# Kernel tuning notes

Hardware: AMD Instinct MI355X
Metric: run time of the kernel (lower is better)

## Reference

```python
import jax, jax.numpy as jnp
import numpy as np
import math

B, H_IM, W_IM, HDIM, HEADS, PS = 16, 56, 56, 512, 8, 7


def setup_inputs() -> dict:
    key = jax.random.key(0)
    ks = jax.random.split(key, 4)
    x = jax.random.normal(ks[0], (B, H_IM * W_IM, HDIM), jnp.float32)
    mask = jnp.zeros((1, 1, H_IM, W_IM), jnp.bool_)
    Wqkv = jax.random.normal(ks[1], (HDIM, 3 * HDIM), jnp.float32) * 0.02
    Wproj = jax.random.normal(ks[2], (HDIM, HDIM), jnp.float32) * 0.02
    bproj = jnp.zeros((HDIM,), jnp.float32)
    rel_bias = jax.random.normal(ks[3], (HEADS, PS * PS, PS * PS), jnp.float32) * 0.02
    return {"x": x, "mask": mask, "Wqkv": Wqkv, "Wproj": Wproj,
            "bproj": bproj, "rel_bias": rel_bias, "H": H_IM, "W": W_IM}


def reference(x, mask, Wqkv, Wproj, bproj, rel_bias, H, W):
    b = x.shape[0]
    ps, g, hd = PS, HEADS, HDIM
    dh = hd // g
    scale = dh ** (-0.5)

    qkv = x @ Wqkv                                   # [b, H*W, 3*hd]
    qkv = qkv.reshape(b, H, W, 3 * hd)
    pad_b = int(math.ceil(H / ps)) * ps - H
    pad_r = int(math.ceil(W / ps)) * ps - W
    qkv = jnp.pad(qkv, ((0, 0), (0, pad_b), (0, pad_r), (0, 0)))
    kmask = jnp.pad(mask, ((0, 0), (0, 0), (0, pad_b), (0, pad_r)), constant_values=True)
    Hp, Wp = H + pad_b, W + pad_r
    sh, sw = Hp // ps, Wp // ps
    K, P = ps * ps, sh * sw

    # patchify: b (sh kh) (sw kw) c -> b (kh kw) (sh sw) c
    qkv = qkv.reshape(b, sh, ps, sw, ps, 3 * hd).transpose(0, 2, 4, 1, 3, 5).reshape(b, K, P, 3 * hd)
    kmask = kmask.reshape(1, 1, sh, ps, sw, ps).transpose(0, 1, 3, 5, 2, 4).reshape(1, 1, K, P)

    qkv = qkv.reshape(b, K, P, 3, g, dh)
    q, k, v = qkv[:, :, :, 0], qkv[:, :, :, 1], qkv[:, :, :, 2]  # each [b, K, P, g, dh]

    attn = jnp.einsum('bqpgc,bkpgc->bgqkp', q, k)    # [b, g, K, K, P]
    attn = (attn + rel_bias[None, :, :, :, None]) * scale
    m = kmask[:, None]                                # [1, 1, 1, K, P]
    attn = jnp.where(m, -jnp.inf, attn)
    attn = jax.nn.softmax(attn, axis=-2)              # softmax over key positions within window
    attn = jnp.where(m, 0.0, attn)

    out = jnp.einsum('bgqkp,bkpgc->bqpgc', attn, v)
    out = out.reshape(b, K, P, hd)
    # un-patchify: b (kh kw) (sh sw) c -> b (sh kh) (sw kw) c
    out = out.reshape(b, ps, ps, sh, sw, hd).transpose(0, 3, 1, 4, 2, 5).reshape(b, Hp, Wp, hd)
    out = out[:, :H, :W, :].reshape(b, H * W, hd)
    return out @ Wproj + bproj
```

## Files before the change

kernel.cpp:

```cpp
#include <hip/hip_runtime.h>
#include <hip/hip_bf16.h>

using bf16 = __hip_bfloat16;
using bf16x8 = __attribute__((ext_vector_type(8))) short;
using f32x4  = __attribute__((ext_vector_type(4))) float;

#define B_    16
#define HIM   56
#define WIM   56
#define HD    512
#define NHEAD 8
#define DH    64
#define NTOK  (HIM*WIM)
#define M_    (B_*NTOK)
#define K49   49

__device__ __forceinline__ void gload_lds16(const void* g, void* l) {
  __builtin_amdgcn_global_load_lds(
      (__attribute__((address_space(1))) const void*)g,
      (__attribute__((address_space(3))) void*)l, 16, 0, 0);
}

__global__ __launch_bounds__(256) void cvt_x_kernel(const float* __restrict__ in,
                                                    bf16* __restrict__ out) {
  size_t i = ((size_t)blockIdx.x * 256 + threadIdx.x) * 8;
  float4 a = *(const float4*)(in + i);
  float4 b = *(const float4*)(in + i + 4);
  union { uint4 v; bf16 h[8]; } o;
  o.h[0] = __float2bfloat16(a.x); o.h[1] = __float2bfloat16(a.y);
  o.h[2] = __float2bfloat16(a.z); o.h[3] = __float2bfloat16(a.w);
  o.h[4] = __float2bfloat16(b.x); o.h[5] = __float2bfloat16(b.y);
  o.h[6] = __float2bfloat16(b.z); o.h[7] = __float2bfloat16(b.w);
  *(uint4*)(out + i) = o.v;
}

__global__ __launch_bounds__(256) void cvt_transpose_kernel(const float* __restrict__ in,
                                                            bf16* __restrict__ out,
                                                            int K, int N) {
  int idx = blockIdx.x * 256 + threadIdx.x;
  int k = idx / N, n = idx - k * N;
  out[(size_t)n * K + k] = __float2bfloat16(in[idx]);
}

template<int N, bool OUT_BF16, bool BIAS>
__global__ __launch_bounds__(512, 2) void gemm8p_kernel(
    const bf16* __restrict__ A,
    const bf16* __restrict__ Bt,
    void* __restrict__ Cp,
    const float* __restrict__ bias,
    int NBX)
{
  constexpr int K = 512;
  __shared__ alignas(16) bf16 lds[2][4][256 * 32];
  const int tid  = threadIdx.x;
  const int lane = tid & 63, wid = tid >> 6;
  const int l15  = lane & 15, kq = lane >> 4;
  const int wm   = wid >> 2,  wn = wid & 3;
  const int cpx = gridDim.x >> 3;
  const int wg  = (blockIdx.x & 7) * cpx + (blockIdx.x >> 3);
  const int by  = wg / NBX, bx = wg - by * NBX;
  const long arow0 = (long)by * 256;
  const long bcol0 = (long)bx * 256;

  auto stageHalf = [&](int ab, int j) {
    const bf16* g = (ab ? Bt + bcol0 * K : A + arow0 * K) + j * 32;
    bf16* lb = &lds[ab][j & 3][0];
#pragma unroll
    for (int c = 0; c < 2; ++c) {
      int s   = c * 512 + tid;
      int row = s >> 2, sl = s & 3;
      int gs  = sl ^ ((row >> 1) & 3);
      gload_lds16((const char*)(g + (long)row * K) + gs * 16,
                  lb + (c * 512 + wid * 64) * 8);
    }
  };
  auto rdA = [&](int slot, int mt) -> bf16x8 {
    int rr = wm * 128 + mt * 16 + l15;
    return *(const bf16x8*)&lds[0][slot][rr * 32 + ((kq ^ ((rr >> 1) & 3)) << 3)];
  };
  auto rdB = [&](int slot, int nt) -> bf16x8 {
    int rr = wn * 64 + nt * 16 + l15;
    return *(const bf16x8*)&lds[1][slot][rr * 32 + ((kq ^ ((rr >> 1) & 3)) << 3)];
  };

  f32x4 acc[8][4] = {};
  bf16x8 af[8], bfA[4], bfB[4];

  stageHalf(0, 0); stageHalf(1, 0);
  stageHalf(0, 1); stageHalf(1, 1);
  stageHalf(0, 2); stageHalf(1, 2);
  asm volatile("s_waitcnt vmcnt(4)" ::: "memory");
  __builtin_amdgcn_s_barrier();
#pragma unroll
  for (int nt = 0; nt < 4; ++nt) bfA[nt] = rdB(0, nt);

#define KS(SLOT, NSLOT, BFC, BFN, JST, DOST, PRE, VMSTR) {                    \
    _Pragma("unroll")                                                         \
    for (int mt = 0; mt < 8; ++mt) af[mt] = rdA(SLOT, mt);                    \
    if (DOST) stageHalf(0, JST);                                              \
    __builtin_amdgcn_s_barrier();                                             \
    __builtin_amdgcn_s_setprio(1);                                            \
    _Pragma("unroll")                                                         \
    for (int mt = 0; mt < 8; ++mt) {                                          \
      acc[mt][0] = __builtin_amdgcn_mfma_f32_16x16x32_bf16(BFC[0], af[mt],    \
                                                           acc[mt][0], 0,0,0);\
      acc[mt][1] = __builtin_amdgcn_mfma_f32_16x16x32_bf16(BFC[1], af[mt],    \
                                                           acc[mt][1], 0,0,0);\
    }                                                                         \
    __builtin_amdgcn_s_setprio(0);                                            \
    if (DOST) stageHalf(1, JST);                                              \
    __builtin_amdgcn_s_setprio(1);                                            \
    _Pragma("unroll")                                                         \
    for (int mt = 0; mt < 8; ++mt) {                                          \
      acc[mt][2] = __builtin_amdgcn_mfma_f32_16x16x32_bf16(BFC[2], af[mt],    \
                                                           acc[mt][2], 0,0,0);\
      acc[mt][3] = __builtin_amdgcn_mfma_f32_16x16x32_bf16(BFC[3], af[mt],    \
                                                           acc[mt][3], 0,0,0);\
    }                                                                         \
    __builtin_amdgcn_s_setprio(0);                                            \
    if (PRE) {                                                                \
      _Pragma("unroll")                                                       \
      for (int nt = 0; nt < 4; ++nt) BFN[nt] = rdB(NSLOT, nt);                \
    }                                                                         \
    asm volatile("s_waitcnt vmcnt(" VMSTR ")" ::: "memory");                  \
    __builtin_amdgcn_s_barrier();                                             \
  }

#pragma unroll 1
  for (int jo = 0; jo < 12; jo += 4) {
    KS(0, 1, bfA, bfB, jo + 3, 1, 1, "4");
    KS(1, 2, bfB, bfA, jo + 4, 1, 1, "4");
    KS(2, 3, bfA, bfB, jo + 5, 1, 1, "4");
    KS(3, 0, bfB, bfA, jo + 6, 1, 1, "4");
  }
  KS(0, 1, bfA, bfB, 15, 1, 1, "4");
  KS(1, 2, bfB, bfA, 0,  0, 1, "0");
  KS(2, 3, bfA, bfB, 0,  0, 1, "0");
  KS(3, 0, bfB, bfA, 0,  0, 0, "0");
#undef KS

  const long crow0 = arow0 + wm * 128;
  const long ccol0 = bcol0 + wn * 64 + kq * 4;
#pragma unroll
  for (int mt = 0; mt < 8; ++mt) {
    long row = crow0 + mt * 16 + l15;
#pragma unroll
    for (int nt = 0; nt < 4; ++nt) {
      long col = ccol0 + nt * 16;
      if (OUT_BF16) {
        union { unsigned long long u; unsigned short h[4]; } pk;
#pragma unroll
        for (int r = 0; r < 4; ++r) {
          bf16 hh = __float2bfloat16(acc[mt][nt][r]);
          pk.h[r] = *(unsigned short*)&hh;
        }
        __builtin_nontemporal_store(pk.u,
            (unsigned long long*)((bf16*)Cp + row * N + col));
      } else {
        f32x4 o = acc[mt][nt];
        if (BIAS) {
          o[0] += bias[col];     o[1] += bias[col + 1];
          o[2] += bias[col + 2]; o[3] += bias[col + 3];
        }
        __builtin_nontemporal_store(o, (f32x4*)((float*)Cp + row * N + col));
      }
    }
  }
}

__global__ __launch_bounds__(256) void attn_win_kernel(
    const bf16* __restrict__ qkv, const float* __restrict__ rb, bf16* __restrict__ outa)
{
  __shared__ alignas(16) bf16 Qs[64 * 72];
  __shared__ alignas(16) bf16 Ks[64 * 72];
  __shared__ alignas(16) bf16 Vt[64 * 72];
  __shared__ alignas(16) bf16 Ps[64 * 72];
  const int tid = threadIdx.x, lane = tid & 63, wid = tid >> 6;
  const int p = blockIdx.x, g = blockIdx.y, b = blockIdx.z;
  const int sh = p >> 3, sw = p & 7;
  const size_t nb = (size_t)b * NTOK;
  const int c8 = (tid & 7) * 8;

#pragma unroll
  for (int it = 0; it < 2; ++it) {
    int t = (tid >> 3) + it * 32;
    uint4 vq = {0, 0, 0, 0}, vk = vq, vv = vq;
    if (t < K49) {
      int ph = t / 7, pw = t - ph * 7;
      int n = (sh * 7 + ph) * WIM + sw * 7 + pw;
      const bf16* src = qkv + (nb + n) * 1536 + g * 64 + c8;
      vq = *(const uint4*)(src);
      vk = *(const uint4*)(src + 512);
      vv = *(const uint4*)(src + 1024);
    }
    *(uint4*)&Qs[t * 72 + c8] = vq;
    *(uint4*)&Ks[t * 72 + c8] = vk;
    union { uint4 u; unsigned short s[8]; } uv; uv.u = vv;
    unsigned short* vt16 = (unsigned short*)Vt;
#pragma unroll
    for (int e = 0; e < 8; ++e) vt16[(c8 + e) * 72 + t] = uv.s[e];
  }
  __syncthreads();

  const int l15 = lane & 15, kq = lane >> 4;
  bf16x8 aq[2];
#pragma unroll
  for (int kk = 0; kk < 2; ++kk)
    aq[kk] = *(const bf16x8*)&Qs[(wid * 16 + l15) * 72 + kk * 32 + kq * 8];
  float sv[4][4];
#pragma unroll
  for (int ct = 0; ct < 4; ++ct) {
    f32x4 acc = {0.f, 0.f, 0.f, 0.f};
#pragma unroll
    for (int kk = 0; kk < 2; ++kk) {
      bf16x8 bk = *(const bf16x8*)&Ks[(ct * 16 + l15) * 72 + kk * 32 + kq * 8];
      acc = __builtin_amdgcn_mfma_f32_16x16x32_bf16(aq[kk], bk, acc, 0, 0, 0);
    }
    int kcol = ct * 16 + l15;
#pragma unroll
    for (int r = 0; r < 4; ++r) {
      int q = wid * 16 + kq * 4 + r;
      float bias = (q < K49 && kcol < K49) ? rb[((size_t)g * K49 + q) * K49 + kcol] : 0.f;
      float v = (acc[r] + bias) * 0.125f;
      sv[ct][r] = (kcol < K49) ? v : -1e30f;
    }
  }
#pragma unroll
  for (int r = 0; r < 4; ++r) {
    float m = fmaxf(fmaxf(sv[0][r], sv[1][r]), fmaxf(sv[2][r], sv[3][r]));
#pragma unroll
    for (int d = 1; d < 16; d <<= 1) m = fmaxf(m, __shfl_xor(m, d));
    float e0 = __expf(sv[0][r] - m), e1 = __expf(sv[1][r] - m);
    float e2 = __expf(sv[2][r] - m), e3 = __expf(sv[3][r] - m);
    float s = e0 + e1 + e2 + e3;
#pragma unroll
    for (int d = 1; d < 16; d <<= 1) s += __shfl_xor(s, d);
    float inv = 1.0f / s;
    int q = wid * 16 + kq * 4 + r;
    Ps[q * 72 +  0 + l15] = __float2bfloat16(e0 * inv);
    Ps[q * 72 + 16 + l15] = __float2bfloat16(e1 * inv);
    Ps[q * 72 + 32 + l15] = __float2bfloat16(e2 * inv);
    Ps[q * 72 + 48 + l15] = __float2bfloat16(e3 * inv);
  }
  __syncthreads();
  bf16x8 ap[2];
#pragma unroll
  for (int kk = 0; kk < 2; ++kk)
    ap[kk] = *(const bf16x8*)&Ps[(wid * 16 + l15) * 72 + kk * 32 + kq * 8];
  f32x4 accO[4] = {};
#pragma unroll
  for (int ct = 0; ct < 4; ++ct)
#pragma unroll
    for (int kk = 0; kk < 2; ++kk) {
      bf16x8 bv = *(const bf16x8*)&Vt[(ct * 16 + l15) * 72 + kk * 32 + kq * 8];
      accO[ct] = __builtin_amdgcn_mfma_f32_16x16x32_bf16(bv, ap[kk], accO[ct], 0, 0, 0);
    }
  int q = wid * 16 + l15;
  if (q < K49) {
    int ph = q / 7, pw = q - ph * 7;
    bf16* dst = outa + (nb + (sh * 7 + ph) * WIM + sw * 7 + pw) * HD + g * 64 + kq * 4;
#pragma unroll
    for (int ct = 0; ct < 4; ++ct) {
      union { unsigned long long u; unsigned short h[4]; } pk;
#pragma unroll
      for (int r = 0; r < 4; ++r) {
        bf16 hh = __float2bfloat16(accO[ct][r]);
        pk.h[r] = *(unsigned short*)&hh;
      }
      *(unsigned long long*)(dst + ct * 16) = pk.u;
    }
  }
}

extern "C" void kernel_launch(void* const* d_in, const int* in_sizes, int n_in,
                              void* d_out, int out_size, void* d_ws, size_t ws_size,
                              hipStream_t stream) {
  (void)in_sizes; (void)n_in; (void)out_size;
  const float* x     = (const float*)d_in[0];
  const float* wqkv  = (const float*)d_in[2];
  const float* wproj = (const float*)d_in[3];
  const float* bproj = (const float*)d_in[4];
  const float* rb    = (const float*)d_in[5];

  char* ws = (char*)d_ws;
  bf16* x_bf    = (bf16*)(ws);
  bf16* wqkv_t  = (bf16*)(ws + 51380224);
  bf16* wproj_t = (bf16*)(ws + 52953088);
  bf16* qkv     = (bf16*)(ws + 53477376);
  bf16* attno   = x_bf;
  float* out    = (float*)d_out;
  if (ws_size < 207618048) return;

  cvt_x_kernel<<<dim3(12544), 256, 0, stream>>>(x, x_bf);
  cvt_transpose_kernel<<<dim3(3072), 256, 0, stream>>>(wqkv, wqkv_t, 512, 1536);
  cvt_transpose_kernel<<<dim3(1024), 256, 0, stream>>>(wproj, wproj_t, 512, 512);
  gemm8p_kernel<1536, true, false><<<dim3(1176), 512, 0, stream>>>(
      x_bf, wqkv_t, (void*)qkv, nullptr, 6);
  attn_win_kernel<<<dim3(64, NHEAD, B_), 256, 0, stream>>>(qkv, rb, attno);
  gemm8p_kernel<512, false, true><<<dim3(392), 512, 0, stream>>>(
      attno, wproj_t, (void*)out, bproj, 2);
}
```

Measured before the change: 255.4 us.

## Shrink GEMM tile to 128x256 with B operand loaded directly from global

Replaces the 256x256 8-wave GEMM with a 128x256 4-wave kernel. Only the A tile is staged through LDS, and each wave reads its own 64-column B slice straight from global into registers, double-buffered across k-steps. This is meant to halve LDS traffic and footprint, allow more blocks per CU, and double the grid for better load balance. In exchange B is no longer shared through LDS, so global and L2 traffic for the weights rises and the load latency is hidden only by register prefetch.

```diff
diff --git a/kernel.cpp b/kernel.cpp
--- a/kernel.cpp
+++ b/kernel.cpp
@@ -43,7 +43,7 @@
 }
 
 template<int N, bool OUT_BF16, bool BIAS>
-__global__ __launch_bounds__(512, 2) void gemm8p_kernel(
+__global__ __launch_bounds__(256, 2) void gemm_bl2_kernel(
     const bf16* __restrict__ A,
     const bf16* __restrict__ Bt,
     void* __restrict__ Cp,
@@ -51,99 +51,83 @@
     int NBX)
 {
   constexpr int K = 512;
-  __shared__ alignas(16) bf16 lds[2][4][256 * 32];
+  __shared__ alignas(16) bf16 ldsA[4][128 * 32];
   const int tid  = threadIdx.x;
   const int lane = tid & 63, wid = tid >> 6;
   const int l15  = lane & 15, kq = lane >> 4;
-  const int wm   = wid >> 2,  wn = wid & 3;
   const int cpx = gridDim.x >> 3;
   const int wg  = (blockIdx.x & 7) * cpx + (blockIdx.x >> 3);
   const int by  = wg / NBX, bx = wg - by * NBX;
-  const long arow0 = (long)by * 256;
+  const long arow0 = (long)by * 128;
   const long bcol0 = (long)bx * 256;
 
-  auto stageHalf = [&](int ab, int j) {
-    const bf16* g = (ab ? Bt + bcol0 * K : A + arow0 * K) + j * 32;
-    bf16* lb = &lds[ab][j & 3][0];
+  auto stageA = [&](int j) {
+    const bf16* g = A + arow0 * K + j * 32;
+    bf16* lb = &ldsA[j & 3][0];
 #pragma unroll
     for (int c = 0; c < 2; ++c) {
-      int s   = c * 512 + tid;
+      int s   = c * 256 + tid;
       int row = s >> 2, sl = s & 3;
       int gs  = sl ^ ((row >> 1) & 3);
       gload_lds16((const char*)(g + (long)row * K) + gs * 16,
-                  lb + (c * 512 + wid * 64) * 8);
+                  lb + (c * 256 + wid * 64) * 8);
     }
   };
   auto rdA = [&](int slot, int mt) -> bf16x8 {
-    int rr = wm * 128 + mt * 16 + l15;
-    return *(const bf16x8*)&lds[0][slot][rr * 32 + ((kq ^ ((rr >> 1) & 3)) << 3)];
+    int rr = mt * 16 + l15;
+    return *(const bf16x8*)&ldsA[slot][rr * 32 + ((kq ^ ((rr >> 1) & 3)) << 3)];
   };
-  auto rdB = [&](int slot, int nt) -> bf16x8 {
-    int rr = wn * 64 + nt * 16 + l15;
-    return *(const bf16x8*)&lds[1][slot][rr * 32 + ((kq ^ ((rr >> 1) & 3)) << 3)];
-  };
+  const bf16* Bbase = Bt + (bcol0 + wid * 64 + l15) * (long)K + kq * 8;
 
   f32x4 acc[8][4] = {};
-  bf16x8 af[8], bfA[4], bfB[4];
-
-  stageHalf(0, 0); stageHalf(1, 0);
-  stageHalf(0, 1); stageHalf(1, 1);
-  stageHalf(0, 2); stageHalf(1, 2);
-  asm volatile("s_waitcnt vmcnt(4)" ::: "memory");
-  __builtin_amdgcn_s_barrier();
-#pragma unroll
-  for (int nt = 0; nt < 4; ++nt) bfA[nt] = rdB(0, nt);
-
-#define KS(SLOT, NSLOT, BFC, BFN, JST, DOST, PRE, VMSTR) {                    \
+  bf16x8 bf0[4], bf1[4];
+
+  stageA(0); stageA(1); stageA(2);
+#pragma unroll
+  for (int nt = 0; nt < 4; ++nt) bf0[nt] = *(const bf16x8*)(Bbase + (long)nt * 16 * K);
+  asm volatile("" ::: "memory");
+#pragma unroll
+  for (int nt = 0; nt < 4; ++nt) bf1[nt] = *(const bf16x8*)(Bbase + (long)nt * 16 * K + 32);
+
+#define KS(SLOT, BF, VM, DOST, JST, DOLD, JLD) {                              \
+    asm volatile("s_waitcnt vmcnt(" VM ")" ::: "memory");                     \
+    __builtin_amdgcn_s_barrier();                                             \
+    bf16x8 af[8];                                                             \
     _Pragma("unroll")                                                         \
     for (int mt = 0; mt < 8; ++mt) af[mt] = rdA(SLOT, mt);                    \
-    if (DOST) stageHalf(0, JST);                                              \
-    __builtin_amdgcn_s_barrier();                                             \
+    if (DOST) stageA(JST);                                                    \
     __builtin_amdgcn_s_setprio(1);                                            \
     _Pragma("unroll")                                                         \
-    for (int mt = 0; mt < 8; ++mt) {                                          \
-      acc[mt][0] = __builtin_amdgcn_mfma_f32_16x16x32_bf16(BFC[0], af[mt],    \
-                                                           acc[mt][0], 0,0,0);\
-      acc[mt][1] = __builtin_amdgcn_mfma_f32_16x16x32_bf16(BFC[1], af[mt],    \
-                                                           acc[mt][1], 0,0,0);\
+    for (int mt = 0; mt < 8; ++mt)                                            \
+      _Pragma("unroll")                                                       \
+      for (int nt = 0; nt < 4; ++nt)                                          \
+        acc[mt][nt] = __builtin_amdgcn_mfma_f32_16x16x32_bf16(BF[nt], af[mt], \
+                                                              acc[mt][nt], 0, 0, 0); \
+    __builtin_amdgcn_s_setprio(0);                                            \
+    if (DOLD) {                                                               \
+      _Pragma("unroll")                                                       \
+      for (int nt = 0; nt < 4; ++nt)                                          \
+        BF[nt] = *(const bf16x8*)(Bbase + (long)nt * 16 * K + (JLD) * 32);    \
     }                                                                         \
-    __builtin_amdgcn_s_setprio(0);                                            \
-    if (DOST) stageHalf(1, JST);                                              \
-    __builtin_amdgcn_s_setprio(1);                                            \
-    _Pragma("unroll")                                                         \
-    for (int mt = 0; mt < 8; ++mt) {                                          \
-      acc[mt][2] = __builtin_amdgcn_mfma_f32_16x16x32_bf16(BFC[2], af[mt],    \
-                                                           acc[mt][2], 0,0,0);\
-      acc[mt][3] = __builtin_amdgcn_mfma_f32_16x16x32_bf16(BFC[3], af[mt],    \
-                                                           acc[mt][3], 0,0,0);\
-    }                                                                         \
-    __builtin_amdgcn_s_setprio(0);                                            \
-    if (PRE) {                                                                \
-      _Pragma("unroll")                                                       \
-      for (int nt = 0; nt < 4; ++nt) BFN[nt] = rdB(NSLOT, nt);                \
-    }                                                                         \
-    asm volatile("s_waitcnt vmcnt(" VMSTR ")" ::: "memory");                  \
-    __builtin_amdgcn_s_barrier();                                             \
-  }
-
+  }
+
+  KS(0, bf0, "4", 1, 3, 1, 2);
 #pragma unroll 1
-  for (int jo = 0; jo < 12; jo += 4) {
-    KS(0, 1, bfA, bfB, jo + 3, 1, 1, "4");
-    KS(1, 2, bfB, bfA, jo + 4, 1, 1, "4");
-    KS(2, 3, bfA, bfB, jo + 5, 1, 1, "4");
-    KS(3, 0, bfB, bfA, jo + 6, 1, 1, "4");
-  }
-  KS(0, 1, bfA, bfB, 15, 1, 1, "4");
-  KS(1, 2, bfB, bfA, 0,  0, 1, "0");
-  KS(2, 3, bfA, bfB, 0,  0, 1, "0");
-  KS(3, 0, bfB, bfA, 0,  0, 0, "0");
+  for (int jo = 1; jo <= 9; jo += 4) {
+    KS(1, bf1, "6", 1, jo + 3, 1, jo + 2);
+    KS(2, bf0, "6", 1, jo + 4, 1, jo + 3);
+    KS(3, bf1, "6", 1, jo + 5, 1, jo + 4);
+    KS(0, bf0, "6", 1, jo + 6, 1, jo + 5);
+  }
+  KS(1, bf1, "6", 0, 0, 1, 15);
+  KS(2, bf0, "4", 0, 0, 0, 0);
+  KS(3, bf1, "0", 0, 0, 0, 0);
 #undef KS
 
-  const long crow0 = arow0 + wm * 128;
-  const long ccol0 = bcol0 + wn * 64 + kq * 4;
+  const long ccol0 = bcol0 + wid * 64 + kq * 4;
 #pragma unroll
   for (int mt = 0; mt < 8; ++mt) {
-    long row = crow0 + mt * 16 + l15;
+    long row = arow0 + mt * 16 + l15;
 #pragma unroll
     for (int nt = 0; nt < 4; ++nt) {
       long col = ccol0 + nt * 16;
@@ -294,9 +278,9 @@
   cvt_x_kernel<<<dim3(12544), 256, 0, stream>>>(x, x_bf);
   cvt_transpose_kernel<<<dim3(3072), 256, 0, stream>>>(wqkv, wqkv_t, 512, 1536);
   cvt_transpose_kernel<<<dim3(1024), 256, 0, stream>>>(wproj, wproj_t, 512, 512);
-  gemm8p_kernel<1536, true, false><<<dim3(1176), 512, 0, stream>>>(
+  gemm_bl2_kernel<1536, true, false><<<dim3(2352), 256, 0, stream>>>(
       x_bf, wqkv_t, (void*)qkv, nullptr, 6);
   attn_win_kernel<<<dim3(64, NHEAD, B_), 256, 0, stream>>>(qkv, rb, attno);
-  gemm8p_kernel<512, false, true><<<dim3(392), 512, 0, stream>>>(
+  gemm_bl2_kernel<512, false, true><<<dim3(784), 256, 0, stream>>>(
       attno, wproj_t, (void*)out, bproj, 2);
 }
```

New measurement: 281.0 us. +10.0%, slower.
